# Optimization experiments

Hardware: AMD Instinct MI355X
Metric: run time of the kernel (lower is better)

## Reference

```python
import jax, jax.numpy as jnp
import numpy as np

MAX_FRAMES = 1000

def _sigmoid_factors(factor, shift, n=MAX_FRAMES):
    x = np.arange(n, dtype=np.float32)
    a = np.clip(x * factor - shift, -80.0, 80.0)
    return jnp.asarray(1.9 / (1.0 + np.exp(a)) + 0.4, dtype=jnp.float32)

F_FACTORS = _sigmoid_factors(1.0, 1.0)  # f_factor=1.0, f_discount=1.0

def setup_inputs() -> dict:
    key = jax.random.key(0)
    k1, _ = jax.random.split(key)
    B, T, D = 32, 1000, 512
    data = jax.random.normal(k1, (B, T, D), dtype=jnp.float32)
    threshold = jnp.full((1,), 30.0, dtype=jnp.float32)  # agent.linear_threshold
    return {"data": data, "threshold": threshold}

def _forward_single(data, thr):
    # data: [T, D]. avg_rep=False, overlapping=False path of forward_single.
    T, D = data.shape
    pref = jnp.cumsum(data, axis=0)  # pref[i-1] = sum(data[:i])
    idx = jnp.arange(1, T)

    def step(carry, xs):
        rep, f_i, ind, start_sum = carry  # rep=data[ind], start_sum=sum(data[:ind])
        i, frame, csum_i = xs             # csum_i = sum(data[:i])
        dist = jnp.linalg.norm(rep - frame)
        boundary = dist > thr * F_FACTORS[jnp.minimum(f_i, MAX_FRAMES - 1)]
        seg_len = (i - ind).astype(data.dtype)
        mean = (csum_i - start_sum) / seg_len  # data[ind:i].mean(0)
        new_rep = jnp.where(boundary, frame, rep)
        new_f = jnp.where(boundary, 0, f_i + 1)
        new_ind = jnp.where(boundary, i, ind)
        new_start = jnp.where(boundary, csum_i, start_sum)
        out_mean = jnp.where(boundary, mean, jnp.zeros_like(mean))
        return (new_rep, new_f, new_ind, new_start), (boundary, out_mean)

    init = (data[0], jnp.int32(0), jnp.int32(0), jnp.zeros((D,), data.dtype))
    _, (flags, means) = jax.lax.scan(step, init, (idx, data[1:], pref[:-1]))
    # Fixed-shape padded result: means[t] is valid iff flags[t] (torch version
    # stacks only the valid rows; final `and False` tail-append is dead code).
    return means, flags

def reference(data, threshold):
    thr = threshold[0]
    means, flags = jax.vmap(_forward_single, in_axes=(0, None))(data, thr)
    return means, flags  # [B, T-1, D] padded segment means, [B, T-1] validity mask
```

## Files before the change

### kernel.cpp

```cpp
#include <hip/hip_runtime.h>
#include <math.h>


typedef float v4 __attribute__((ext_vector_type(4)));

#define T_F    1000
#define D_DIM  512
#define NV4    128
#define BAND_W 4
#define RUNB   16
#define RPBB   63

__device__ __forceinline__ float wave_sum64(float x) {
  x += __shfl_xor(x, 1);
  x += __shfl_xor(x, 2);
  x += __shfl_xor(x, 4);
  x += __shfl_xor(x, 8);
  x += __shfl_xor(x, 16);
  x += __shfl_xor(x, 32);
  return x;
}

__device__ __forceinline__ v4 sel4(bool c, v4 a, v4 b) {
  v4 r;
  r.x = c ? a.x : b.x; r.y = c ? a.y : b.y;
  r.z = c ? a.z : b.z; r.w = c ? a.w : b.w;
  return r;
}

__global__ __launch_bounds__(256)
void band_kernel(const float* __restrict__ data, const float* __restrict__ thrp,
                 unsigned char* __restrict__ deltab, int B) {
  const int lane = threadIdx.x & 63;
  const int wid  = threadIdx.x >> 6;
  const int run  = blockIdx.x * 4 + wid;
  if (run >= B * RPBB) return;
  const int b   = run / RPBB;
  const int s0i = (run % RPBB) * RUNB;

  const v4* __restrict__ dp = reinterpret_cast<const v4*>(data) + (size_t)b * T_F * NV4;
  unsigned char* __restrict__ dbp = deltab + (size_t)b * 1024;

  const int   wl  = lane & 3;
  const float thr = thrp[0];
  float Ff  = 1.9f / (1.0f + expf((float)wl - 1.0f)) + 0.4f;
  float tt  = thr * Ff;
  const float tf2l = tt * tt;

  const int q0 = lane, q1 = 64 + lane;
  v4 ra[8], rb[8];
#pragma unroll
  for (int d = 0; d < 8; ++d) {
    int t = s0i + d; if (t > T_F - 1) t = T_F - 1;
    ra[d] = dp[(size_t)t * NV4 + q0];
    rb[d] = dp[(size_t)t * NV4 + q1];
  }

  v4 pna[3], pnb[3];
  unsigned long long packed = 0ull;

#pragma unroll
  for (int u = 0; u < RUNB; ++u) {
    const int s  = s0i + u;
    const int su = u & 7;
    float p[BAND_W];
#pragma unroll
    for (int w = 0; w < BAND_W; ++w) {
      const int sj = (u + 1 + w) & 7;
      v4 d0 = ra[su] - ra[sj];
      v4 d1 = rb[su] - rb[sj];
      p[w] = d0.x*d0.x + d0.y*d0.y + d0.z*d0.z + d0.w*d0.w
           + d1.x*d1.x + d1.y*d1.y + d1.z*d1.z + d1.w*d1.w;
    }
    if (u >= 3 && (u - 3) < RUNB - 4) {
      const int cs = (u + 5) & 7;
      ra[cs] = pna[u % 3];
      rb[cs] = pnb[u % 3];
    }
    if (u < RUNB - 4) {
      int tn = s + 8; if (tn > T_F - 1) tn = T_F - 1;
      pna[u % 3] = dp[(size_t)tn * NV4 + q0];
      pnb[u % 3] = dp[(size_t)tn * NV4 + q1];
    }

#pragma unroll
    for (int w = 0; w < BAND_W; ++w) {
      p[w] += __shfl_xor(p[w], 1);
      p[w] += __shfl_xor(p[w], 2);
      p[w] += __shfl_xor(p[w], 4);
    }
    const bool bt0 = (lane & 1) != 0, bt1 = (lane & 2) != 0;
    float q0v  = bt0 ? p[1] : p[0];
    float q1v  = bt0 ? p[3] : p[2];
    float comb = bt1 ? q1v : q0v;
    comb += __shfl_xor(comb, 8);
    comb += __shfl_xor(comb, 16);
    comb += __shfl_xor(comb, 32);
    bool valid = (s + 1 + wl) <= (T_F - 1);
    bool bnd   = valid && (comb > tf2l);
    unsigned long long m = __ballot(bnd);
    unsigned long long delta =
        (unsigned long long)__ffsll((unsigned long long)(m & 0xFull));
    packed |= delta << (4 * u);
  }
  if (lane == 0)
    *reinterpret_cast<unsigned long long*>(dbp + (s0i >> 1)) = packed;
}

__global__ __launch_bounds__(256)
void meanscan_kernel(const float* __restrict__ data,
                     const float* __restrict__ thrp,
                     const unsigned char* __restrict__ deltab,
                     float* __restrict__ out, int B) {
  const int lane = threadIdx.x & 63;
  const int wv   = threadIdx.x >> 6;
  const int b    = blockIdx.y;
  const int X    = blockIdx.x * 16;
  const int i0   = X + wv * 4;

  const v4* __restrict__ dp  = reinterpret_cast<const v4*>(data) + (size_t)b * T_F * NV4;
  v4* __restrict__ mp        = reinterpret_cast<v4*>(out) + (size_t)b * (T_F - 1) * NV4;
  float* __restrict__ fl     = out + (size_t)B * (T_F - 1) * D_DIM + (size_t)b * (T_F - 1);
  const int q0 = lane, q1 = 64 + lane;

  __shared__ int so_l[16];

  if (wv == 0) {
    if (lane < 16) so_l[lane] = -1;
    const uint2 dd = reinterpret_cast<const uint2*>(deltab + (size_t)b * 1024)[lane];
    unsigned plo = dd.x;
    unsigned phi = dd.y;

    int s = 0;
    bool need_exact = false;
    const int lim = X + 16;
    while (s < T_F - 1 && s < lim) {
      unsigned lo = (unsigned)__builtin_amdgcn_readlane((int)plo, s >> 4);
      unsigned hi = (unsigned)__builtin_amdgcn_readlane((int)phi, s >> 4);
      unsigned word = (s & 8) ? hi : lo;
      int delta = (word >> ((s & 7) * 4)) & 15;
      if (delta == 0) { need_exact = (s < T_F - 1 - BAND_W); break; }
      int ns = s + delta;
      if (ns >= X && ns < lim && lane == 0) so_l[ns - X] = s;
      s = ns;
    }

    if (need_exact) {
      const float thr = thrp[0];
      int ind = s, f = 0;
      v4 rep0 = dp[(size_t)ind * NV4 + q0];
      v4 rep1 = dp[(size_t)ind * NV4 + q1];
      int iend = X + 15; if (iend > T_F - 1) iend = T_F - 1;
      for (int i = s + 1; i <= iend; ++i) {
        float av = fminf((float)f - 1.0f, 80.0f);
        float Ff = 1.9f / (1.0f + expf(av)) + 0.4f;
        float t2 = thr * Ff; t2 *= t2;
        v4 x0 = dp[(size_t)i * NV4 + q0];
        v4 x1 = dp[(size_t)i * NV4 + q1];
        v4 d0 = rep0 - x0, d1 = rep1 - x1;
        float part = d0.x*d0.x + d0.y*d0.y + d0.z*d0.z + d0.w*d0.w
                   + d1.x*d1.x + d1.y*d1.y + d1.z*d1.z + d1.w*d1.w;
        float d2 = wave_sum64(part);
        bool bnd = d2 > t2;
        if (bnd) {
          if (i >= X && lane == 0) so_l[i - X] = ind;
          ind = i; f = 0; rep0 = x0; rep1 = x1;
        } else {
          f += 1;
        }
      }
    }
  }
  __syncthreads();

  const v4 z = {0.f, 0.f, 0.f, 0.f};
#pragma unroll
  for (int q = 0; q < 4; ++q) {
    const int i = i0 + q;
    if (i < 1 || i > T_F - 1) continue;
    const int s = so_l[wv * 4 + q];
    if (s < 0) {
      __builtin_nontemporal_store(z, &mp[(size_t)(i - 1) * NV4 + q0]);
      __builtin_nontemporal_store(z, &mp[(size_t)(i - 1) * NV4 + q1]);
      if (lane == 0) __builtin_nontemporal_store(0.0f, &fl[i - 1]);
      continue;
    }
    const int len = i - s;
    v4 a0 = z, a1 = z;
    if (len <= BAND_W) {
#pragma unroll
      for (int j = 0; j < BAND_W; ++j) {
        const int t = (j < len) ? (s + j) : (i - 1);
        const float msk = (j < len) ? 1.0f : 0.0f;
        v4 x0 = dp[(size_t)t * NV4 + q0];
        v4 x1 = dp[(size_t)t * NV4 + q1];
        a0.x += x0.x * msk; a0.y += x0.y * msk; a0.z += x0.z * msk; a0.w += x0.w * msk;
        a1.x += x1.x * msk; a1.y += x1.y * msk; a1.z += x1.z * msk; a1.w += x1.w * msk;
      }
    } else {
      for (int t = s; t < i; ++t) {
        a0 += dp[(size_t)t * NV4 + q0];
        a1 += dp[(size_t)t * NV4 + q1];
      }
    }
    const float inv = 1.0f / (float)len;
    a0.x *= inv; a0.y *= inv; a0.z *= inv; a0.w *= inv;
    a1.x *= inv; a1.y *= inv; a1.z *= inv; a1.w *= inv;
    __builtin_nontemporal_store(a0, &mp[(size_t)(i - 1) * NV4 + q0]);
    __builtin_nontemporal_store(a1, &mp[(size_t)(i - 1) * NV4 + q1]);
    if (lane == 0) __builtin_nontemporal_store(1.0f, &fl[i - 1]);
  }
}

__global__ __launch_bounds__(64, 1)
void dist_agg_mono(const float* __restrict__ data,
                   const float* __restrict__ thrp,
                   float* __restrict__ out, int B) {
  const int b    = blockIdx.x;
  const int lane = threadIdx.x;
  const float thr = thrp[0];
  const v4* __restrict__ dp = reinterpret_cast<const v4*>(data) + (size_t)b * T_F * NV4;
  v4* __restrict__ mp       = reinterpret_cast<v4*>(out) + (size_t)b * (T_F - 1) * NV4;
  float* __restrict__ fp    = out + (size_t)B * (T_F - 1) * D_DIM + (size_t)b * (T_F - 1);
  const int s0 = lane, s1 = 64 + lane;

  v4 rep0 = dp[s0], rep1 = dp[s1];
  v4 cs0  = rep0,  cs1  = rep1;
  v4 ss0  = {0.f,0.f,0.f,0.f}, ss1 = {0.f,0.f,0.f,0.f};
  int ind = 0, fi = 0;
  const float F0     = 1.9f / (1.0f + expf(-1.0f)) + 0.4f;
  const float tf0    = thr * F0;
  const float tf2_f0 = tf0 * tf0;
  float tf2 = tf2_f0;

  for (int i = 1; i < T_F; ++i) {
    float an      = fminf((float)fi, 80.0f);
    float Fn      = 1.9f / (1.0f + expf(an)) + 0.4f;
    float tn      = thr * Fn;
    float tf2_inc = tn * tn;
    v4 fa = dp[(size_t)i * NV4 + s0];
    v4 fb = dp[(size_t)i * NV4 + s1];
    v4 d0 = rep0 - fa, d1 = rep1 - fb;
    float part = d0.x*d0.x + d0.y*d0.y + d0.z*d0.z + d0.w*d0.w
               + d1.x*d1.x + d1.y*d1.y + d1.z*d1.z + d1.w*d1.w;
    float dist2 = wave_sum64(part);
    bool bnd = dist2 > tf2;
    float inv = 1.0f / (float)(i - ind);
    v4 df0 = cs0 - ss0, df1 = cs1 - ss1;
    v4 m0, m1, z = {0.f,0.f,0.f,0.f};
    m0.x = df0.x*inv; m0.y = df0.y*inv; m0.z = df0.z*inv; m0.w = df0.w*inv;
    m1.x = df1.x*inv; m1.y = df1.y*inv; m1.z = df1.z*inv; m1.w = df1.w*inv;
    mp[(size_t)(i-1) * NV4 + s0] = sel4(bnd, m0, z);
    mp[(size_t)(i-1) * NV4 + s1] = sel4(bnd, m1, z);
    if (lane == 0) fp[i-1] = bnd ? 1.0f : 0.0f;
    rep0 = sel4(bnd, fa, rep0); rep1 = sel4(bnd, fb, rep1);
    ss0  = sel4(bnd, cs0, ss0); ss1  = sel4(bnd, cs1, ss1);
    ind  = bnd ? i : ind;
    fi   = bnd ? 0 : fi + 1;
    tf2  = bnd ? tf2_f0 : tf2_inc;
    cs0 += fa; cs1 += fb;
  }
}

extern "C" void kernel_launch(void* const* d_in, const int* in_sizes, int n_in,
                              void* d_out, int out_size, void* d_ws, size_t ws_size,
                              hipStream_t stream) {
  const float* data = (const float*)d_in[0];
  const float* thr  = (const float*)d_in[1];
  float* out        = (float*)d_out;
  const int B = in_sizes[0] / (T_F * D_DIM);

  const size_t need = (size_t)B * 1024;

  if (ws_size >= need) {
    unsigned char* deltab = (unsigned char*)d_ws;
    const int runs = B * RPBB;
    band_kernel<<<(runs + 3) / 4, 256, 0, stream>>>(data, thr, deltab, B);
    meanscan_kernel<<<dim3(63, B), 256, 0, stream>>>(data, thr, deltab, out, B);
  } else {
    dist_agg_mono<<<B, 64, 0, stream>>>(data, thr, out, B);
  }
}
```

Baseline: 147.3 us.

## Use single-wave blocks in meanscan and keep segment lengths in registers

Shrinks meanscan_kernel from four waves to one wave per block. The single wave walks the delta chain and packs the 16 segment lengths into a 64-bit register, so shared memory and __syncthreads are only used on the rare exact-scan path. This removes the block-wide barrier where three waves sat idle while wave 0 walked the chain. In exchange, one wave now does all 16 output rows serially, which cuts parallelism per block (from 4 waves to 1) and may lower latency hiding.

```diff
diff --git a/kernel.cpp b/kernel.cpp
--- a/kernel.cpp
+++ b/kernel.cpp
@@ -107,90 +107,98 @@
     *reinterpret_cast<unsigned long long*>(dbp + (s0i >> 1)) = packed;
 }
 
-__global__ __launch_bounds__(256)
+__global__ __launch_bounds__(64)
 void meanscan_kernel(const float* __restrict__ data,
                      const float* __restrict__ thrp,
                      const unsigned char* __restrict__ deltab,
                      float* __restrict__ out, int B) {
-  const int lane = threadIdx.x & 63;
-  const int wv   = threadIdx.x >> 6;
+  const int lane = threadIdx.x;
   const int b    = blockIdx.y;
   const int X    = blockIdx.x * 16;
-  const int i0   = X + wv * 4;
 
   const v4* __restrict__ dp  = reinterpret_cast<const v4*>(data) + (size_t)b * T_F * NV4;
   v4* __restrict__ mp        = reinterpret_cast<v4*>(out) + (size_t)b * (T_F - 1) * NV4;
   float* __restrict__ fl     = out + (size_t)B * (T_F - 1) * D_DIM + (size_t)b * (T_F - 1);
   const int q0 = lane, q1 = 64 + lane;
 
+  const uint2 dd = reinterpret_cast<const uint2*>(deltab + (size_t)b * 1024)[lane];
+  const unsigned plo = dd.x;
+  const unsigned phi = dd.y;
+
+  unsigned long long lenpack = 0ull;
+  int s = 0;
+  bool need_exact = false;
+  const int lim = X + 16;
+  while (s < T_F - 1 && s < lim) {
+    unsigned lo = (unsigned)__builtin_amdgcn_readlane((int)plo, s >> 4);
+    unsigned hi = (unsigned)__builtin_amdgcn_readlane((int)phi, s >> 4);
+    unsigned word = (s & 8) ? hi : lo;
+    int delta = (word >> ((s & 7) * 4)) & 15;
+    if (delta == 0) { need_exact = (s < T_F - 1 - BAND_W); break; }
+    int ns = s + delta;
+    if (ns >= X && ns < lim)
+      lenpack |= (unsigned long long)delta << (4 * (ns - X));
+    s = ns;
+  }
+
   __shared__ int so_l[16];
-
-  if (wv == 0) {
-    if (lane < 16) so_l[lane] = -1;
-    const uint2 dd = reinterpret_cast<const uint2*>(deltab + (size_t)b * 1024)[lane];
-    unsigned plo = dd.x;
-    unsigned phi = dd.y;
-
-    int s = 0;
-    bool need_exact = false;
-    const int lim = X + 16;
-    while (s < T_F - 1 && s < lim) {
-      unsigned lo = (unsigned)__builtin_amdgcn_readlane((int)plo, s >> 4);
-      unsigned hi = (unsigned)__builtin_amdgcn_readlane((int)phi, s >> 4);
-      unsigned word = (s & 8) ? hi : lo;
-      int delta = (word >> ((s & 7) * 4)) & 15;
-      if (delta == 0) { need_exact = (s < T_F - 1 - BAND_W); break; }
-      int ns = s + delta;
-      if (ns >= X && ns < lim && lane == 0) so_l[ns - X] = s;
-      s = ns;
-    }
-
-    if (need_exact) {
-      const float thr = thrp[0];
-      int ind = s, f = 0;
-      v4 rep0 = dp[(size_t)ind * NV4 + q0];
-      v4 rep1 = dp[(size_t)ind * NV4 + q1];
-      int iend = X + 15; if (iend > T_F - 1) iend = T_F - 1;
-      for (int i = s + 1; i <= iend; ++i) {
-        float av = fminf((float)f - 1.0f, 80.0f);
-        float Ff = 1.9f / (1.0f + expf(av)) + 0.4f;
-        float t2 = thr * Ff; t2 *= t2;
-        v4 x0 = dp[(size_t)i * NV4 + q0];
-        v4 x1 = dp[(size_t)i * NV4 + q1];
-        v4 d0 = rep0 - x0, d1 = rep1 - x1;
-        float part = d0.x*d0.x + d0.y*d0.y + d0.z*d0.z + d0.w*d0.w
-                   + d1.x*d1.x + d1.y*d1.y + d1.z*d1.z + d1.w*d1.w;
-        float d2 = wave_sum64(part);
-        bool bnd = d2 > t2;
-        if (bnd) {
-          if (i >= X && lane == 0) so_l[i - X] = ind;
-          ind = i; f = 0; rep0 = x0; rep1 = x1;
-        } else {
-          f += 1;
-        }
+  if (need_exact) {
+    if (lane < 16) {
+      int d = (int)((lenpack >> (4 * lane)) & 15);
+      so_l[lane] = d ? (X + lane - d) : -1;
+    }
+    __syncthreads();
+    const float thr = thrp[0];
+    int ind = s, f = 0;
+    v4 rep0 = dp[(size_t)ind * NV4 + q0];
+    v4 rep1 = dp[(size_t)ind * NV4 + q1];
+    int iend = X + 15; if (iend > T_F - 1) iend = T_F - 1;
+    for (int i = s + 1; i <= iend; ++i) {
+      float av = fminf((float)f - 1.0f, 80.0f);
+      float Ff = 1.9f / (1.0f + expf(av)) + 0.4f;
+      float t2 = thr * Ff; t2 *= t2;
+      v4 x0 = dp[(size_t)i * NV4 + q0];
+      v4 x1 = dp[(size_t)i * NV4 + q1];
+      v4 d0 = rep0 - x0, d1 = rep1 - x1;
+      float part = d0.x*d0.x + d0.y*d0.y + d0.z*d0.z + d0.w*d0.w
+                 + d1.x*d1.x + d1.y*d1.y + d1.z*d1.z + d1.w*d1.w;
+      float d2 = wave_sum64(part);
+      bool bnd = d2 > t2;
+      if (bnd) {
+        if (i >= X && lane == 0) so_l[i - X] = ind;
+        ind = i; f = 0; rep0 = x0; rep1 = x1;
+      } else {
+        f += 1;
       }
     }
-  }
-  __syncthreads();
+    __syncthreads();
+  }
 
   const v4 z = {0.f, 0.f, 0.f, 0.f};
 #pragma unroll
-  for (int q = 0; q < 4; ++q) {
-    const int i = i0 + q;
+  for (int e = 0; e < 16; ++e) {
+    const int i = X + e;
     if (i < 1 || i > T_F - 1) continue;
-    const int s = so_l[wv * 4 + q];
-    if (s < 0) {
+    int sv, len;
+    if (!need_exact) {
+      len = (int)((lenpack >> (4 * e)) & 15);
+      sv  = i - len;
+      if (len == 0) sv = -1;
+    } else {
+      sv  = so_l[e];
+      len = i - sv;
+    }
+    if (sv < 0) {
       __builtin_nontemporal_store(z, &mp[(size_t)(i - 1) * NV4 + q0]);
       __builtin_nontemporal_store(z, &mp[(size_t)(i - 1) * NV4 + q1]);
       if (lane == 0) __builtin_nontemporal_store(0.0f, &fl[i - 1]);
       continue;
     }
-    const int len = i - s;
     v4 a0 = z, a1 = z;
     if (len <= BAND_W) {
 #pragma unroll
       for (int j = 0; j < BAND_W; ++j) {
-        const int t = (j < len) ? (s + j) : (i - 1);
+        const int t = (j < len) ? (sv + j) : (i - 1);
         const float msk = (j < len) ? 1.0f : 0.0f;
         v4 x0 = dp[(size_t)t * NV4 + q0];
         v4 x1 = dp[(size_t)t * NV4 + q1];
@@ -198,7 +206,7 @@
         a1.x += x1.x * msk; a1.y += x1.y * msk; a1.z += x1.z * msk; a1.w += x1.w * msk;
       }
     } else {
-      for (int t = s; t < i; ++t) {
+      for (int t = sv; t < i; ++t) {
         a0 += dp[(size_t)t * NV4 + q0];
         a1 += dp[(size_t)t * NV4 + q1];
       }
@@ -276,7 +284,7 @@
     unsigned char* deltab = (unsigned char*)d_ws;
     const int runs = B * RPBB;
     band_kernel<<<(runs + 3) / 4, 256, 0, stream>>>(data, thr, deltab, B);
-    meanscan_kernel<<<dim3(63, B), 256, 0, stream>>>(data, thr, deltab, out, B);
+    meanscan_kernel<<<dim3(63, B), 64, 0, stream>>>(data, thr, deltab, out, B);
   } else {
     dist_agg_mono<<<B, 64, 0, stream>>>(data, thr, out, B);
   }
```

Result: slower. 152.2 us (+3.3%).
